# Optimization experiments

Hardware: AMD Instinct MI355X
Metric: run time of the kernel (lower is better)

The kernel has to match this reference:

```python
import jax, jax.numpy as jnp
import numpy as np

# edge types from metadata: (src_type, 'to', dst_type)
NODE_SRC = [0, 1, 2, 3, 0, 1, 2, 1, 3, 1]
NODE_DST = [0, 1, 2, 3, 1, 0, 1, 2, 1, 3]
N_NODES = 30000
N_EDGES = 400000
HEADS1 = 8


def _han_conv(xs, edges, proj_W, proj_b, att_src, att_dst, k_W, k_b, q, heads):
    """Faithful port of torch_geometric HANConv (eval mode, dropout off)."""
    out_ch = proj_W.shape[-1]
    D = out_ch // heads
    N = xs[0].shape[0]
    # per-node-type projection -> [N, H, D]
    h = [(xs[t] @ proj_W[t] + proj_b[t]).reshape(N, heads, D) for t in range(4)]
    outs = {t: [] for t in range(4)}
    for e in range(10):
        s, d = NODE_SRC[e], NODE_DST[e]
        row, col = edges[e, 0], edges[e, 1]
        a_src = (h[s] * att_src[e]).sum(-1)  # [N, H]
        a_dst = (h[d] * att_dst[e]).sum(-1)  # [N, H]
        alpha = jax.nn.leaky_relu(a_src[row] + a_dst[col], 0.2)  # [E, H]
        # segment softmax over incoming edges of each dst node
        amax = jax.ops.segment_max(alpha, col, num_segments=N)
        ex = jnp.exp(alpha - amax[col])
        denom = jax.ops.segment_sum(ex, col, num_segments=N)
        w = ex / (denom[col] + 1e-16)
        msg = h[s][row] * w[:, :, None]  # [E, H, D]
        agg = jax.ops.segment_sum(msg, col, num_segments=N).reshape(N, out_ch)
        outs[d].append(jax.nn.relu(agg))
    # semantic-level attention fusion across relations ending at each node type
    res = []
    for t in range(4):
        stk = jnp.stack(outs[t])  # [M, N, C]
        score = (q * jnp.tanh(stk @ k_W + k_b).mean(axis=1)).sum(-1)  # [M]
        sattn = jax.nn.softmax(score)
        res.append((sattn[:, None, None] * stk).sum(0))  # [N, C]
    return res


def setup_inputs() -> dict:
    key = jax.random.key(0)
    ks = jax.random.split(key, 24)
    inp = {}
    for t in range(4):
        inp[f"x{t}"] = jax.random.normal(ks[t], (N_NODES, 256), dtype=jnp.float32)
    inp["edges"] = jax.random.randint(ks[4], (10, 2, N_EDGES), 0, N_NODES, dtype=jnp.int32)
    s = 0.05
    inp["proj1_W"] = jax.random.normal(ks[5], (4, 256, 128), dtype=jnp.float32) * s
    inp["proj1_b"] = jax.random.normal(ks[6], (4, 128), dtype=jnp.float32) * s
    inp["att1_src"] = jax.random.normal(ks[7], (10, 8, 16), dtype=jnp.float32) * s
    inp["att1_dst"] = jax.random.normal(ks[8], (10, 8, 16), dtype=jnp.float32) * s
    inp["k1_W"] = jax.random.normal(ks[9], (128, 128), dtype=jnp.float32) * s
    inp["k1_b"] = jax.random.normal(ks[10], (128,), dtype=jnp.float32) * s
    inp["q1"] = jax.random.normal(ks[11], (128,), dtype=jnp.float32) * s
    inp["proj2_W"] = jax.random.normal(ks[12], (4, 128, 32), dtype=jnp.float32) * s
    inp["proj2_b"] = jax.random.normal(ks[13], (4, 32), dtype=jnp.float32) * s
    inp["att2_src"] = jax.random.normal(ks[14], (10, 1, 32), dtype=jnp.float32) * s
    inp["att2_dst"] = jax.random.normal(ks[15], (10, 1, 32), dtype=jnp.float32) * s
    inp["k2_W"] = jax.random.normal(ks[16], (32, 32), dtype=jnp.float32) * s
    inp["k2_b"] = jax.random.normal(ks[17], (32,), dtype=jnp.float32) * s
    inp["q2"] = jax.random.normal(ks[18], (32,), dtype=jnp.float32) * s
    return inp


def reference(x0, x1, x2, x3, edges,
              proj1_W, proj1_b, att1_src, att1_dst, k1_W, k1_b, q1,
              proj2_W, proj2_b, att2_src, att2_dst, k2_W, k2_b, q2):
    # eval mode: all F.dropout calls are identity
    xs = [x0, x1, x2, x3]
    h = _han_conv(xs, edges, proj1_W, proj1_b, att1_src, att1_dst, k1_W, k1_b, q1, HEADS1)
    h = [jax.nn.elu(v) for v in h]
    o = _han_conv(h, edges, proj2_W, proj2_b, att2_src, att2_dst, k2_W, k2_b, q2, 1)
    # final per-node softmax over channel dim for each node type; stack since all N equal
    return jnp.stack([jax.nn.softmax(v, axis=1) for v in o])  # [4, N, 32]
```

## Files before the change

### kernel.cpp

```cpp
#include <hip/hip_runtime.h>
#include <hip/hip_fp16.h>

#define NN 30000
#define NE 400000
#define NBUCK 59
#define BPR 98
#define EPB 4096
#define CAPREG 12288
#define BCAP 12288

__constant__ int d_SRC[10] = {0,1,2,3,0,1,2,1,3,1};
__constant__ int d_DST[10] = {0,1,2,3,1,0,1,2,1,3};
__constant__ int d_RORD[10] = {1,5,7,9,0,4,2,6,3,8};
__constant__ int d_FCNT[4] = {2,4,2,2};
__constant__ int d_FREL[4][4] = {{0,5,0,0},{1,4,6,8},{2,7,0,0},{3,9,0,0}};

__constant__ int d_XRELA[8]  = {0,4,2,6,8,1,5,7};
__constant__ int d_XBASEA[8] = {0,1875,3750,5625,0,1875,3750,5625};
__constant__ int d_XCNTA[8]  = {7500,5625,3750,1875,7500,5625,3750,1875};
__constant__ int d_XRELB[8]  = {4,2,6,3,1,5,7,9};

typedef _Float16 f16x8 __attribute__((ext_vector_type(8)));
typedef float f32x4 __attribute__((ext_vector_type(4)));

struct __attribute__((aligned(8))) h2x2 { __half2 a, b; };

template<int BN, bool AF16>
__global__ __launch_bounds__(256)
void mgemm_k(const float* __restrict__ A, long sA,
             const float* __restrict__ B, long sB,
             const float* __restrict__ bias, long sBias,
             float* __restrict__ C, long sC,
             int M, int K, int N, int relu_a, int epi)
{
    constexpr int BM = 128, BK = 32, MR = 2;
    constexpr int NF = BN / 16;
    constexpr int LDK = BK + 8;
    const int z = blockIdx.z;
    const _Float16* __restrict__ Ah = (const _Float16*)A;
    if constexpr (AF16) Ah += (long)z * sA; else A += (long)z * sA;
    B += (long)z * sB;
    bias += (long)z * sBias;
    C += (long)z * sC;
    const int m0 = blockIdx.x * BM;
    const int n0 = blockIdx.y * BN;
    const int tid = threadIdx.x;
    const int wv = tid >> 6;
    const int l  = tid & 63;
    const int fm = l & 15;
    const int fg = l >> 4;

    __shared__ _Float16 As[BM][LDK];
    __shared__ _Float16 Bs[BN][LDK];
    __shared__ float red[4][BN];

    f32x4 acc[MR][NF];
#pragma unroll
    for (int mr = 0; mr < MR; ++mr)
#pragma unroll
        for (int f = 0; f < NF; ++f) acc[mr][f] = (f32x4){0.f, 0.f, 0.f, 0.f};

    const int arow = tid >> 1;
    const int akc  = (tid & 1) << 4;
    const int grow = m0 + arow;

    for (int k0 = 0; k0 < K; k0 += BK) {
        f16x8 ap0, ap1;
        if (grow < M) {
            if constexpr (AF16) {
                const _Float16* aq = Ah + (long)grow * K + k0 + akc;
                ap0 = *(const f16x8*)aq;
                ap1 = *(const f16x8*)(aq + 8);
                if (relu_a) {
#pragma unroll
                    for (int j = 0; j < 8; ++j) {
                        ap0[j] = ap0[j] > (_Float16)0.f ? ap0[j] : (_Float16)0.f;
                        ap1[j] = ap1[j] > (_Float16)0.f ? ap1[j] : (_Float16)0.f;
                    }
                }
            } else {
                const float* aq = A + (long)grow * K + k0 + akc;
                float4 u0 = *(const float4*)aq;
                float4 u1 = *(const float4*)(aq + 4);
                float4 u2 = *(const float4*)(aq + 8);
                float4 u3 = *(const float4*)(aq + 12);
                float v[16] = {u0.x,u0.y,u0.z,u0.w, u1.x,u1.y,u1.z,u1.w,
                               u2.x,u2.y,u2.z,u2.w, u3.x,u3.y,u3.z,u3.w};
                if (relu_a) {
#pragma unroll
                    for (int j = 0; j < 16; ++j) v[j] = fmaxf(v[j], 0.f);
                }
#pragma unroll
                for (int j = 0; j < 8; ++j) { ap0[j] = (_Float16)v[j]; ap1[j] = (_Float16)v[j+8]; }
            }
        } else {
#pragma unroll
            for (int j = 0; j < 8; ++j) { ap0[j] = (_Float16)0.f; ap1[j] = (_Float16)0.f; }
        }
        *(f16x8*)&As[arow][akc]     = ap0;
        *(f16x8*)&As[arow][akc + 8] = ap1;

        if constexpr (BN == 64) {
            const int bk = tid >> 4;
            const int bn = (tid & 15) << 2;
#pragma unroll
            for (int kk = 0; kk < 2; ++kk) {
                int kr = bk + kk * 16;
                float4 u = *(const float4*)(B + (long)(k0 + kr) * N + n0 + bn);
                Bs[bn + 0][kr] = (_Float16)u.x;
                Bs[bn + 1][kr] = (_Float16)u.y;
                Bs[bn + 2][kr] = (_Float16)u.z;
                Bs[bn + 3][kr] = (_Float16)u.w;
            }
        } else {
            const int bk = tid >> 3;
            const int bn = (tid & 7) << 2;
            float4 u = *(const float4*)(B + (long)(k0 + bk) * N + n0 + bn);
            Bs[bn + 0][bk] = (_Float16)u.x;
            Bs[bn + 1][bk] = (_Float16)u.y;
            Bs[bn + 2][bk] = (_Float16)u.z;
            Bs[bn + 3][bk] = (_Float16)u.w;
        }
        __syncthreads();

        f16x8 a0 = *(const f16x8*)&As[wv * 32 + fm][fg * 8];
        f16x8 a1 = *(const f16x8*)&As[wv * 32 + 16 + fm][fg * 8];
#pragma unroll
        for (int f = 0; f < NF; ++f) {
            f16x8 b = *(const f16x8*)&Bs[f * 16 + fm][fg * 8];
            acc[0][f] = __builtin_amdgcn_mfma_f32_16x16x32_f16(a0, b, acc[0][f], 0, 0, 0);
            acc[1][f] = __builtin_amdgcn_mfma_f32_16x16x32_f16(a1, b, acc[1][f], 0, 0, 0);
        }
        __syncthreads();
    }

    if (epi == 0) {
#pragma unroll
        for (int f = 0; f < NF; ++f) {
            float bz = bias[n0 + f * 16 + fm];
#pragma unroll
            for (int mr = 0; mr < MR; ++mr)
#pragma unroll
                for (int i = 0; i < 4; ++i) {
                    int gr = m0 + wv * 32 + mr * 16 + fg * 4 + i;
                    if (gr < M) C[(long)gr * N + n0 + f * 16 + fm] = acc[mr][f][i] + bz;
                }
        }
    } else if (epi == 2) {
        __half* Ch = (__half*)C;
#pragma unroll
        for (int f = 0; f < NF; ++f) {
            float bz = bias[n0 + f * 16 + fm];
#pragma unroll
            for (int mr = 0; mr < MR; ++mr)
#pragma unroll
                for (int i = 0; i < 4; ++i) {
                    int gr = m0 + wv * 32 + mr * 16 + fg * 4 + i;
                    if (gr < M) Ch[(long)gr * N + n0 + f * 16 + fm] = __float2half(acc[mr][f][i] + bz);
                }
        }
    } else {
#pragma unroll
        for (int f = 0; f < NF; ++f) {
            float bz = bias[n0 + f * 16 + fm];
            float s = 0.f;
#pragma unroll
            for (int mr = 0; mr < MR; ++mr)
#pragma unroll
                for (int i = 0; i < 4; ++i) {
                    int gr = m0 + wv * 32 + mr * 16 + fg * 4 + i;
                    if (gr < M) s += tanhf(acc[mr][f][i] + bz);
                }
            s += __shfl_xor(s, 16, 64);
            s += __shfl_xor(s, 32, 64);
            if (fg == 0) red[wv][f * 16 + fm] = s;
        }
        __syncthreads();
        if (tid < BN) {
            float s = red[0][tid] + red[1][tid] + red[2][tid] + red[3][tid];
            unsafeAtomicAdd(&C[n0 + tid], s);
        }
    }
}

__global__ __launch_bounds__(256)
void init_bincur(int* __restrict__ binCur)
{
    int i = blockIdx.x * 256 + threadIdx.x;
    if (i < 10 * NBUCK) binCur[i] = (i % NBUCK) * CAPREG;
}

__global__ __launch_bounds__(256)
void csr_binA(const int* __restrict__ edges, int* __restrict__ binCur,
              unsigned* __restrict__ binned)
{
    __shared__ int lcnt[NBUCK];
    __shared__ int gbase[NBUCK];
    int rel = blockIdx.x / BPR;
    int blk = blockIdx.x - rel * BPR;
    int base = blk * EPB;
    int tid = threadIdx.x;
    for (int b = tid; b < NBUCK; b += 256) lcnt[b] = 0;
    __syncthreads();
    const int* er = edges + (long)rel * 2 * NE;
    const int* ec = er + NE;
    unsigned pk[16];
    unsigned mt[16];
#pragma unroll
    for (int k = 0; k < 16; ++k) {
        int i = base + k * 256 + tid;
        if (i < NE) {
            int r = er[i];
            int c = ec[i];
            int b = c >> 9;
            int lo = atomicAdd(&lcnt[b], 1);
            pk[k] = ((unsigned)c << 15) | (unsigned)r;
            mt[k] = ((unsigned)b << 16) | (unsigned)lo;
        } else {
            mt[k] = 0xFFFFFFFFu;
        }
    }
    __syncthreads();
    if (tid < NBUCK) gbase[tid] = atomicAdd(&binCur[rel * NBUCK + tid], lcnt[tid]);
    __syncthreads();
    unsigned* bn = binned + (long)rel * NBUCK * CAPREG;
#pragma unroll
    for (int k = 0; k < 16; ++k) {
        if (mt[k] != 0xFFFFFFFFu) {
            int b = mt[k] >> 16;
            int lo = mt[k] & 0xFFFF;
            bn[gbase[b] + lo] = pk[k];
        }
    }
}

__global__ __launch_bounds__(64)
void bucket_scan(const int* __restrict__ binCur, int* __restrict__ bbase,
                 int* __restrict__ off_all)
{
    int rel = blockIdx.x;
    int t = threadIdx.x;
    __shared__ int c[64];
    int v = (t < NBUCK) ? (binCur[rel * NBUCK + t] - t * CAPREG) : 0;
    c[t] = v;
    __syncthreads();
    for (int d = 1; d < 64; d <<= 1) {
        int u = (t >= d) ? c[t - d] : 0;
        __syncthreads();
        c[t] += u;
        __syncthreads();
    }
    if (t < NBUCK) bbase[rel * NBUCK + t] = c[t] - v;
    if (t == 0) off_all[rel * (NN + 1) + NN] = NE;
}

__global__ __launch_bounds__(256)
void csr_binB(const int* __restrict__ binCur, const int* __restrict__ bbase,
              const unsigned* __restrict__ binned,
              int* __restrict__ off_all, unsigned short* __restrict__ rows)
{
    __shared__ int cntS[512];
    __shared__ int lcur[512];
    __shared__ int part[256];
    __shared__ int buf[BCAP];
    int rel = blockIdx.x / NBUCK;
    int bkt = blockIdx.x - rel * NBUCK;
    const unsigned* bn = binned + ((long)rel * NBUCK + bkt) * CAPREG;
    int* off = off_all + rel * (NN + 1);
    unsigned short* rw = rows + (long)rel * NE;
    int cnt = binCur[rel * NBUCK + bkt] - bkt * CAPREG;
    int gbase = bbase[rel * NBUCK + bkt];
    int nb0 = bkt << 9;
    int nb1 = min(nb0 + 512, NN);
    int nloc = nb1 - nb0;
    int tid = threadIdx.x;

    cntS[tid] = 0; cntS[tid + 256] = 0;
    __syncthreads();
    for (int j = tid; j < cnt; j += 256) {
        int c = (int)(bn[j] >> 15);
        atomicAdd(&cntS[c - nb0], 1);
    }
    __syncthreads();
    int c0 = cntS[2 * tid], c1 = cntS[2 * tid + 1];
    part[tid] = c0 + c1;
    __syncthreads();
    for (int d = 1; d < 256; d <<= 1) {
        int u = (tid >= d) ? part[tid - d] : 0;
        __syncthreads();
        part[tid] += u;
        __syncthreads();
    }
    int pre = (tid == 0) ? 0 : part[tid - 1];
    cntS[2 * tid] = pre;
    cntS[2 * tid + 1] = pre + c0;
    __syncthreads();
    for (int i = tid; i < nloc; i += 256) off[nb0 + i] = gbase + cntS[i];
    lcur[tid] = cntS[tid]; lcur[tid + 256] = cntS[tid + 256];
    __syncthreads();
    if (cnt <= BCAP) {
        for (int j = tid; j < cnt; j += 256) {
            unsigned p = bn[j];
            int r = (int)(p & 0x7FFF);
            int c = (int)(p >> 15);
            int pos = atomicAdd(&lcur[c - nb0], 1);
            buf[pos] = r;
        }
        __syncthreads();
        for (int i = tid; i < cnt; i += 256) rw[gbase + i] = (unsigned short)buf[i];
    } else {
        for (int j = tid; j < cnt; j += 256) {
            unsigned p = bn[j];
            int r = (int)(p & 0x7FFF);
            int c = (int)(p >> 15);
            int pos = atomicAdd(&lcur[c - nb0], 1);
            rw[gbase + pos] = (unsigned short)r;
        }
    }
}

__global__ __launch_bounds__(256)
void attn_dots1(const __half* __restrict__ h1h,
                const float* __restrict__ att_src,
                const float* __restrict__ att_dst,
                float* __restrict__ asrc, float* __restrict__ adst)
{
    int gid = blockIdx.x * 256 + threadIdx.x;
    int wave = gid >> 6;
    int lane = gid & 63;
    if (wave >= 4 * NN) return;
    int t = wave / NN;
    int n = wave - t * NN;
    __half2 hh = *(const __half2*)&h1h[(long)(t * NN + n) * 128 + 2 * lane];
    float2 hv = __half22float2(hh);
    const int SRCc[10] = {0,1,2,3,0,1,2,1,3,1};
    const int DSTc[10] = {0,1,2,3,1,0,1,2,1,3};
#pragma unroll
    for (int e = 0; e < 10; ++e) {
        if (SRCc[e] == t) {
            float2 av = *(const float2*)&att_src[e * 128 + 2 * lane];
            float p = hv.x * av.x + hv.y * av.y;
#pragma unroll
            for (int off = 1; off < 8; off <<= 1) p += __shfl_xor(p, off, 64);
            if ((lane & 7) == 0) asrc[(long)(e * NN + n) * 8 + (lane >> 3)] = p;
        }
        if (DSTc[e] == t) {
            float2 bv = *(const float2*)&att_dst[e * 128 + 2 * lane];
            float p = hv.x * bv.x + hv.y * bv.y;
#pragma unroll
            for (int off = 1; off < 8; off <<= 1) p += __shfl_xor(p, off, 64);
            if ((lane & 7) == 0) adst[(long)(e * NN + n) * 8 + (lane >> 3)] = p;
        }
    }
}

__global__ __launch_bounds__(256)
void gather_agg1_all(const int* __restrict__ csr_off,
                     const unsigned short* __restrict__ csr_rows,
                     const float* __restrict__ asrc1, const float* __restrict__ adst1,
                     const __half* __restrict__ h1h, __half* __restrict__ slots16)
{
    int g = blockIdx.x;
    int xcd = g & 7;
    int slot = g >> 3;
    int e, i;
    if (slot < d_XCNTA[xcd]) { e = d_XRELA[xcd]; i = d_XBASEA[xcd] + slot; }
    else                     { e = d_XRELB[xcd]; i = slot - d_XCNTA[xcd]; }
    int node = i * 4 + (threadIdx.x >> 6);
    int lane = threadIdx.x & 63;
    if (node >= NN) return;
    const int* off = csr_off + e * (NN + 1);
    const unsigned short* rows = csr_rows + (long)e * NE;
    const float* asrc_e = asrc1 + (long)e * NN * 8;
    const float* adst_e = adst1 + (long)e * NN * 8;
    const _Float16* h1s = (const _Float16*)h1h + (long)d_SRC[e] * NN * 128;
    __half* out = slots16 + (long)e * NN * 128;

    const int g2  = lane >> 4;
    const int s16 = lane & 15;
    const int hv  = s16 >> 1;
    const int eA  = lane >> 3;
    const int hA  = lane & 7;
    int beg = off[node], end = off[node + 1];
    float adA = adst_e[node * 8 + hA];
    float den = (g2 == 0) ? 1e-16f : 0.f;
    float a0 = 0.f, a1 = 0.f, a2 = 0.f, a3 = 0.f;
    float a4 = 0.f, a5 = 0.f, a6 = 0.f, a7 = 0.f;

#define GA1_STEP(i)                                                              \
    {                                                                            \
        int e0 = 4 * (i) + g2;                                                   \
        float wi = __shfl(w, e0 * 8 + hv, 64);                                   \
        int ri = __shfl(r, e0 * 8, 64);                                          \
        f16x8 v = *(const f16x8*)(h1s + (long)ri * 128 + 8 * s16);               \
        den += wi;                                                               \
        a0 += wi * (float)v[0]; a1 += wi * (float)v[1];                          \
        a2 += wi * (float)v[2]; a3 += wi * (float)v[3];                          \
        a4 += wi * (float)v[4]; a5 += wi * (float)v[5];                          \
        a6 += wi * (float)v[6]; a7 += wi * (float)v[7];                          \
    }

    if (beg < end) {
        int j0 = beg;
        int jj = j0 + eA;
        bool ok = jj < end;
        int r = (int)rows[ok ? jj : beg];
        float aw = asrc_e[r * 8 + hA] + adA;
        while (true) {
            float al = aw > 0.f ? aw : 0.2f * aw;
            float w = ok ? __expf(al) : 0.f;
            int j1 = j0 + 8;
            int rn = r; float awn = 0.f; bool okn = false;
            if (j1 < end) {
                int jn = j1 + eA;
                okn = jn < end;
                rn = (int)rows[okn ? jn : beg];
                awn = asrc_e[rn * 8 + hA] + adA;
            }
            int cnt = end - j0;
            GA1_STEP(0)
            if (cnt > 4) { GA1_STEP(1) }
            if (j1 >= end) break;
            j0 = j1; r = rn; aw = awn; ok = okn;
        }
    }
#undef GA1_STEP
#pragma unroll
    for (int m = 16; m < 64; m <<= 1) {
        a0 += __shfl_xor(a0, m, 64); a1 += __shfl_xor(a1, m, 64);
        a2 += __shfl_xor(a2, m, 64); a3 += __shfl_xor(a3, m, 64);
        a4 += __shfl_xor(a4, m, 64); a5 += __shfl_xor(a5, m, 64);
        a6 += __shfl_xor(a6, m, 64); a7 += __shfl_xor(a7, m, 64);
        den += __shfl_xor(den, m, 64);
    }
    if (g2 == 0) {
        float inv = 1.0f / den;
        f16x8 o;
        o[0] = (_Float16)(a0 * inv); o[1] = (_Float16)(a1 * inv);
        o[2] = (_Float16)(a2 * inv); o[3] = (_Float16)(a3 * inv);
        o[4] = (_Float16)(a4 * inv); o[5] = (_Float16)(a5 * inv);
        o[6] = (_Float16)(a6 * inv); o[7] = (_Float16)(a7 * inv);
        *(f16x8*)((_Float16*)out + (long)node * 128 + 8 * s16) = o;
    }
}

__global__ __launch_bounds__(256)
void fusion_all(const __half* __restrict__ slots16, const float* __restrict__ sattn,
                __half* __restrict__ h1f)
{
    int t = blockIdx.y;
    int idx = blockIdx.x * 256 + threadIdx.x;
    if (idx >= NN * 32) return;
    int c4 = idx & 31;
    int n = idx >> 5;
    long off = (long)n * 128 + c4 * 4;
    int cnt = d_FCNT[t];
    float o0 = 0.f, o1 = 0.f, o2 = 0.f, o3 = 0.f;
    for (int j = 0; j < cnt; ++j) {
        int e = d_FREL[t][j];
        float w = sattn[e];
        const __half* p = slots16 + (long)e * NN * 128 + off;
        float2 v01 = __half22float2(*(const __half2*)p);
        float2 v23 = __half22float2(*(const __half2*)(p + 2));
        o0 += w * fmaxf(v01.x, 0.f);
        o1 += w * fmaxf(v01.y, 0.f);
        o2 += w * fmaxf(v23.x, 0.f);
        o3 += w * fmaxf(v23.y, 0.f);
    }
    o0 = o0 > 0.f ? o0 : __expf(o0) - 1.f;
    o1 = o1 > 0.f ? o1 : __expf(o1) - 1.f;
    o2 = o2 > 0.f ? o2 : __expf(o2) - 1.f;
    o3 = o3 > 0.f ? o3 : __expf(o3) - 1.f;
    __half* q = h1f + (long)t * NN * 128 + off;
    *(__half2*)q = __floats2half2_rn(o0, o1);
    *(__half2*)(q + 2) = __floats2half2_rn(o2, o3);
}

__global__ __launch_bounds__(256)
void attn_dots2(const __half* __restrict__ h2h,
                const float* __restrict__ att_src,
                const float* __restrict__ att_dst,
                float* __restrict__ asrc, float* __restrict__ adst)
{
    int gid = blockIdx.x * 256 + threadIdx.x;
    int p = gid >> 5;
    int l = gid & 31;
    if (p >= 10 * NN) return;
    int e = p / NN, n = p - e * NN;
    int s = d_SRC[e], d = d_DST[e];
    float hs = __half2float(h2h[(long)(s * NN + n) * 32 + l]);
    float hd = __half2float(h2h[(long)(d * NN + n) * 32 + l]);
    float ps = hs * att_src[e * 32 + l];
    float pd = hd * att_dst[e * 32 + l];
#pragma unroll
    for (int off = 1; off < 32; off <<= 1) {
        ps += __shfl_xor(ps, off, 64);
        pd += __shfl_xor(pd, off, 64);
    }
    if (l == 0) { asrc[e * NN + n] = ps; adst[e * NN + n] = pd; }
}

__global__ __launch_bounds__(256)
void gather_agg2(const int* __restrict__ csr_off,
                 const unsigned short* __restrict__ csr_rows,
                 const __half* __restrict__ h2h,
                 const float* __restrict__ asrc, const float* __restrict__ adst,
                 __half* __restrict__ agg2h)
{
    int e = d_RORD[blockIdx.y];
    int node = blockIdx.x * 8 + (threadIdx.x >> 5);
    int lane = threadIdx.x & 31;
    if (node >= NN) return;
    const int* off = csr_off + e * (NN + 1);
    const unsigned short* rows = csr_rows + (long)e * NE;
    const __half* h2s = h2h + (long)d_SRC[e] * NN * 32;
    const float* as = asrc + e * NN;
    const int slot = lane >> 3;
    const int sub = lane & 7;
    float ad = adst[e * NN + node];
    int beg = off[node], end = off[node + 1];
    float den = (slot == 0) ? 1e-16f : 0.f;
    float a0 = 0.f, a1 = 0.f, a2 = 0.f, a3 = 0.f;

#define GA2_STEP(i)                                                              \
    {                                                                            \
        int e0 = (i) * 4 + slot;                                                 \
        float wi = __shfl(w, e0, 32);                                            \
        int ri = __shfl(r, e0, 32);                                              \
        h2x2 v = *(const h2x2*)(h2s + (long)ri * 32 + 4 * sub);                  \
        float2 f0 = __half22float2(v.a);                                         \
        float2 f1 = __half22float2(v.b);                                         \
        den += wi;                                                               \
        a0 += wi * f0.x; a1 += wi * f0.y; a2 += wi * f1.x; a3 += wi * f1.y;      \
    }

    for (int j0 = beg; j0 < end; j0 += 32) {
        int jj = j0 + lane;
        bool ok = jj < end;
        int r = (int)rows[ok ? jj : beg];
        float a = as[r] + ad;
        a = a > 0.f ? a : 0.2f * a;
        float w = ok ? __expf(a) : 0.f;
        int cnt = end - j0;
        if (cnt >= 32) {
            GA2_STEP(0) GA2_STEP(1) GA2_STEP(2) GA2_STEP(3)
            GA2_STEP(4) GA2_STEP(5) GA2_STEP(6) GA2_STEP(7)
        } else {
            int it = (cnt + 3) >> 2;
            for (int i = 0; i < it; ++i) GA2_STEP(i)
        }
    }
#undef GA2_STEP
#pragma unroll
    for (int m = 8; m < 32; m <<= 1) {
        a0 += __shfl_xor(a0, m, 32);
        a1 += __shfl_xor(a1, m, 32);
        a2 += __shfl_xor(a2, m, 32);
        a3 += __shfl_xor(a3, m, 32);
        den += __shfl_xor(den, m, 32);
    }
    if (slot == 0) {
        float inv = 1.0f / den;
        h2x2 o;
        o.a = __floats2half2_rn(a0 * inv, a1 * inv);
        o.b = __floats2half2_rn(a2 * inv, a3 * inv);
        *(h2x2*)(agg2h + ((long)e * NN + node) * 32 + 4 * sub) = o;
    }
}

__global__ void score_all_k(const float* __restrict__ colsum, const float* __restrict__ q,
                            float* __restrict__ sattn, int C)
{
    __shared__ float sc[10];
    int tid = threadIdx.x;
    if (tid < 10) {
        float s = 0.f;
        for (int c = 0; c < C; ++c) s += q[c] * colsum[tid * C + c];
        sc[tid] = s / (float)NN;
    }
    __syncthreads();
    if (tid < 4) {
        float mx = -1e30f;
        for (int m = 0; m < 10; ++m) if (d_DST[m] == tid) mx = fmaxf(mx, sc[m]);
        float ex[10];
        float sum = 0.f;
        for (int m = 0; m < 10; ++m) {
            ex[m] = 0.f;
            if (d_DST[m] == tid) { ex[m] = __expf(sc[m] - mx); sum += ex[m]; }
        }
        for (int m = 0; m < 10; ++m) if (d_DST[m] == tid) sattn[m] = ex[m] / sum;
    }
}

__global__ __launch_bounds__(256)
void final_softmax(const __half* __restrict__ agg, const float* __restrict__ sattn,
                   float* __restrict__ out)
{
    int gid = blockIdx.x * 256 + threadIdx.x;
    int c = gid & 31;
    int p = gid >> 5;
    if (p >= 4 * NN) return;
    int t = p / NN, n = p - t * NN;
    float f = 0.f;
    for (int m = 0; m < 10; ++m) {
        if (d_DST[m] != t) continue;
        f += sattn[m] * fmaxf(__half2float(agg[(long)(m * NN + n) * 32 + c]), 0.f);
    }
    float mx = f;
#pragma unroll
    for (int off = 1; off < 32; off <<= 1) mx = fmaxf(mx, __shfl_xor(mx, off, 64));
    float ex = __expf(f - mx);
    float sm = ex;
#pragma unroll
    for (int off = 1; off < 32; off <<= 1) sm += __shfl_xor(sm, off, 64);
    out[(long)(t * NN + n) * 32 + c] = ex / sm;
}

extern "C" void kernel_launch(void* const* d_in, const int* in_sizes, int n_in,
                              void* d_out, int out_size, void* d_ws, size_t ws_size,
                              hipStream_t stream) {
    const float* x[4] = {
        (const float*)d_in[0], (const float*)d_in[1],
        (const float*)d_in[2], (const float*)d_in[3]};
    const int* edges = (const int*)d_in[4];
    const float* W1    = (const float*)d_in[5];
    const float* b1    = (const float*)d_in[6];
    const float* att1s = (const float*)d_in[7];
    const float* att1d = (const float*)d_in[8];
    const float* k1W   = (const float*)d_in[9];
    const float* k1b   = (const float*)d_in[10];
    const float* q1    = (const float*)d_in[11];
    const float* W2    = (const float*)d_in[12];
    const float* b2    = (const float*)d_in[13];
    const float* att2s = (const float*)d_in[14];
    const float* att2d = (const float*)d_in[15];
    const float* k2W   = (const float*)d_in[16];
    const float* k2b   = (const float*)d_in[17];
    const float* q2    = (const float*)d_in[18];

    float* W = (float*)d_ws;
    __half* h1h    = (__half*)W;
    __half* h1f    = (__half*)W;
    __half* h2h    = (__half*)(W + 7680000);
    __half* slots16 = (__half*)(W + 15360000);
    __half* agg2h  = (__half*)(W + 15360000);
    unsigned* binned = (unsigned*)(W + 15360000);
    int*   binCur  = (int*)(W + 15360000 + 7249920);
    int*   bbase   = binCur + 640;
    float* asrc1   = W + 34560000;
    float* adst1   = W + 36960000;
    float* asrc2   = W + 36960000;
    float* adst2   = W + 37260000;
    float* colsum1 = W + 39360000;
    float* sattn1  = W + 39361280;
    float* colsum2 = W + 39361296;
    float* sattn2  = W + 39361616;
    int*   csr_off = (int*)(W + 39361640);
    unsigned short* csr_row = (unsigned short*)(csr_off + 300016);

    init_bincur<<<3, 256, 0, stream>>>(binCur);
    csr_binA<<<BPR * 10, 256, 0, stream>>>(edges, binCur, binned);
    bucket_scan<<<10, 64, 0, stream>>>(binCur, bbase, csr_off);
    csr_binB<<<NBUCK * 10, 256, 0, stream>>>(binCur, bbase, binned, csr_off, csr_row);

    hipMemsetAsync(colsum1, 0, 1632L * 4, stream);

    for (int t = 0; t < 4; ++t) {
        mgemm_k<64, false><<<dim3(235, 2, 1), 256, 0, stream>>>(
            x[t], 0, W1 + (long)t * 256 * 128, 0, b1 + t * 128, 0,
            (float*)(h1h + (long)t * NN * 128), 0, NN, 256, 128, 0, 2);
    }

    attn_dots1<<<30000, 256, 0, stream>>>(h1h, att1s, att1d, asrc1, adst1);

    gather_agg1_all<<<75000, 256, 0, stream>>>(
        csr_off, csr_row, asrc1, adst1, h1h, slots16);

    mgemm_k<64, true><<<dim3(235, 2, 10), 256, 0, stream>>>(
        (const float*)slots16, (long)NN * 128, k1W, 0, k1b, 0,
        colsum1, 128, NN, 128, 128, 1, 1);
    score_all_k<<<1, 64, 0, stream>>>(colsum1, q1, sattn1, 128);

    fusion_all<<<dim3(3750, 4), 256, 0, stream>>>(slots16, sattn1, h1f);

    mgemm_k<32, true><<<dim3(235, 1, 4), 256, 0, stream>>>(
        (const float*)h1f, (long)NN * 128, W2, 128L * 32, b2, 32,
        (float*)h2h, (long)NN * 16, NN, 128, 32, 0, 2);

    attn_dots2<<<37500, 256, 0, stream>>>(h2h, att2s, att2d, asrc2, adst2);
    gather_agg2<<<dim3(3750, 10), 256, 0, stream>>>(
        csr_off, csr_row, h2h, asrc2, adst2, agg2h);

    mgemm_k<32, true><<<dim3(235, 1, 10), 256, 0, stream>>>(
        (const float*)agg2h, (long)NN * 32, k2W, 0, k2b, 0,
        colsum2, 32L, NN, 32, 32, 1, 1);
    score_all_k<<<1, 64, 0, stream>>>(colsum2, q2, sattn2, 32);
    final_softmax<<<15000, 256, 0, stream>>>(agg2h, sattn2, (float*)d_out);
}
```

Before: 762.3 us.

## Merge setup kernels, batch layer-1 projection, split CSR rows by source half

Several changes land together. The layer-1 projection becomes one batched launch over all four node types instead of four launches. The bucket_scan kernel and the memset are folded into csr_binB and a combined init kernel. CSR rows within each destination are partitioned into low and high source indices, with a split offset stored per node. The layer-1 gather then walks the two segments separately, dropping its software-prefetch loop, presumably to improve locality of the h1 row gathers. This removes several launches, but each csr_binB block now recomputes the prefix sum serially and the gather loses its prefetch overlap.

Result: faster. 728.5 us (-4.4%).

```diff
diff --git a/kernel.cpp b/kernel.cpp
--- a/kernel.cpp
+++ b/kernel.cpp
@@ -8,6 +8,7 @@
 #define EPB 4096
 #define CAPREG 12288
 #define BCAP 12288
+#define HSPLIT 15000
 
 __constant__ int d_SRC[10] = {0,1,2,3,0,1,2,1,3,1};
 __constant__ int d_DST[10] = {0,1,2,3,1,0,1,2,1,3};
@@ -25,9 +26,101 @@
 
 struct __attribute__((aligned(8))) h2x2 { __half2 a, b; };
 
-template<int BN, bool AF16>
-__global__ __launch_bounds__(256)
-void mgemm_k(const float* __restrict__ A, long sA,
+__global__ __launch_bounds__(256)
+void proj1_k(const float* __restrict__ A0, const float* __restrict__ A1,
+             const float* __restrict__ A2, const float* __restrict__ A3,
+             const float* __restrict__ B, const float* __restrict__ bias,
+             __half* __restrict__ C)
+{
+    constexpr int BM = 128, BK = 32, MR = 2, NF = 4, LDK = BK + 8;
+    constexpr int K = 256, N = 128, M = NN;
+    const int z = blockIdx.z;
+    const float* A = (z == 0) ? A0 : (z == 1) ? A1 : (z == 2) ? A2 : A3;
+    const float* Bz = B + (long)z * K * N;
+    const float* bz = bias + z * N;
+    __half* Cz = C + (long)z * M * N;
+    const int m0 = blockIdx.x * BM;
+    const int n0 = blockIdx.y * 64;
+    const int tid = threadIdx.x;
+    const int wv = tid >> 6;
+    const int l  = tid & 63;
+    const int fm = l & 15;
+    const int fg = l >> 4;
+
+    __shared__ _Float16 As[BM][LDK];
+    __shared__ _Float16 Bs[64][LDK];
+
+    f32x4 acc[MR][NF];
+#pragma unroll
+    for (int mr = 0; mr < MR; ++mr)
+#pragma unroll
+        for (int f = 0; f < NF; ++f) acc[mr][f] = (f32x4){0.f, 0.f, 0.f, 0.f};
+
+    const int arow = tid >> 1;
+    const int akc  = (tid & 1) << 4;
+    const int grow = m0 + arow;
+
+    for (int k0 = 0; k0 < K; k0 += BK) {
+        f16x8 ap0, ap1;
+        if (grow < M) {
+            const float* aq = A + (long)grow * K + k0 + akc;
+            float4 u0 = *(const float4*)aq;
+            float4 u1 = *(const float4*)(aq + 4);
+            float4 u2 = *(const float4*)(aq + 8);
+            float4 u3 = *(const float4*)(aq + 12);
+            float v[16] = {u0.x,u0.y,u0.z,u0.w, u1.x,u1.y,u1.z,u1.w,
+                           u2.x,u2.y,u2.z,u2.w, u3.x,u3.y,u3.z,u3.w};
+#pragma unroll
+            for (int j = 0; j < 8; ++j) { ap0[j] = (_Float16)v[j]; ap1[j] = (_Float16)v[j+8]; }
+        } else {
+#pragma unroll
+            for (int j = 0; j < 8; ++j) { ap0[j] = (_Float16)0.f; ap1[j] = (_Float16)0.f; }
+        }
+        *(f16x8*)&As[arow][akc]     = ap0;
+        *(f16x8*)&As[arow][akc + 8] = ap1;
+
+        {
+            const int bk = tid >> 4;
+            const int bn = (tid & 15) << 2;
+#pragma unroll
+            for (int kk = 0; kk < 2; ++kk) {
+                int kr = bk + kk * 16;
+                float4 u = *(const float4*)(Bz + (long)(k0 + kr) * N + n0 + bn);
+                Bs[bn + 0][kr] = (_Float16)u.x;
+                Bs[bn + 1][kr] = (_Float16)u.y;
+                Bs[bn + 2][kr] = (_Float16)u.z;
+                Bs[bn + 3][kr] = (_Float16)u.w;
+            }
+        }
+        __syncthreads();
+
+        f16x8 a0 = *(const f16x8*)&As[wv * 32 + fm][fg * 8];
+        f16x8 a1 = *(const f16x8*)&As[wv * 32 + 16 + fm][fg * 8];
+#pragma unroll
+        for (int f = 0; f < NF; ++f) {
+            f16x8 b = *(const f16x8*)&Bs[f * 16 + fm][fg * 8];
+            acc[0][f] = __builtin_amdgcn_mfma_f32_16x16x32_f16(a0, b, acc[0][f], 0, 0, 0);
+            acc[1][f] = __builtin_amdgcn_mfma_f32_16x16x32_f16(a1, b, acc[1][f], 0, 0, 0);
+        }
+        __syncthreads();
+    }
+
+#pragma unroll
+    for (int f = 0; f < NF; ++f) {
+        float bzv = bz[n0 + f * 16 + fm];
+#pragma unroll
+        for (int mr = 0; mr < MR; ++mr)
+#pragma unroll
+            for (int i = 0; i < 4; ++i) {
+                int gr = m0 + wv * 32 + mr * 16 + fg * 4 + i;
+                if (gr < M) Cz[(long)gr * N + n0 + f * 16 + fm] = __float2half(acc[mr][f][i] + bzv);
+            }
+    }
+}
+
+template<int BN>
+__global__ __launch_bounds__(256)
+void mgemm_k(const _Float16* __restrict__ Ah, long sA,
              const float* __restrict__ B, long sB,
              const float* __restrict__ bias, long sBias,
              float* __restrict__ C, long sC,
@@ -37,8 +130,7 @@
     constexpr int NF = BN / 16;
     constexpr int LDK = BK + 8;
     const int z = blockIdx.z;
-    const _Float16* __restrict__ Ah = (const _Float16*)A;
-    if constexpr (AF16) Ah += (long)z * sA; else A += (long)z * sA;
+    Ah += (long)z * sA;
     B += (long)z * sB;
     bias += (long)z * sBias;
     C += (long)z * sC;
@@ -67,31 +159,15 @@
     for (int k0 = 0; k0 < K; k0 += BK) {
         f16x8 ap0, ap1;
         if (grow < M) {
-            if constexpr (AF16) {
-                const _Float16* aq = Ah + (long)grow * K + k0 + akc;
-                ap0 = *(const f16x8*)aq;
-                ap1 = *(const f16x8*)(aq + 8);
-                if (relu_a) {
-#pragma unroll
-                    for (int j = 0; j < 8; ++j) {
-                        ap0[j] = ap0[j] > (_Float16)0.f ? ap0[j] : (_Float16)0.f;
-                        ap1[j] = ap1[j] > (_Float16)0.f ? ap1[j] : (_Float16)0.f;
-                    }
+            const _Float16* aq = Ah + (long)grow * K + k0 + akc;
+            ap0 = *(const f16x8*)aq;
+            ap1 = *(const f16x8*)(aq + 8);
+            if (relu_a) {
+#pragma unroll
+                for (int j = 0; j < 8; ++j) {
+                    ap0[j] = ap0[j] > (_Float16)0.f ? ap0[j] : (_Float16)0.f;
+                    ap1[j] = ap1[j] > (_Float16)0.f ? ap1[j] : (_Float16)0.f;
                 }
-            } else {
-                const float* aq = A + (long)grow * K + k0 + akc;
-                float4 u0 = *(const float4*)aq;
-                float4 u1 = *(const float4*)(aq + 4);
-                float4 u2 = *(const float4*)(aq + 8);
-                float4 u3 = *(const float4*)(aq + 12);
-                float v[16] = {u0.x,u0.y,u0.z,u0.w, u1.x,u1.y,u1.z,u1.w,
-                               u2.x,u2.y,u2.z,u2.w, u3.x,u3.y,u3.z,u3.w};
-                if (relu_a) {
-#pragma unroll
-                    for (int j = 0; j < 16; ++j) v[j] = fmaxf(v[j], 0.f);
-                }
-#pragma unroll
-                for (int j = 0; j < 8; ++j) { ap0[j] = (_Float16)v[j]; ap1[j] = (_Float16)v[j+8]; }
             }
         } else {
 #pragma unroll
@@ -134,19 +210,7 @@
         __syncthreads();
     }
 
-    if (epi == 0) {
-#pragma unroll
-        for (int f = 0; f < NF; ++f) {
-            float bz = bias[n0 + f * 16 + fm];
-#pragma unroll
-            for (int mr = 0; mr < MR; ++mr)
-#pragma unroll
-                for (int i = 0; i < 4; ++i) {
-                    int gr = m0 + wv * 32 + mr * 16 + fg * 4 + i;
-                    if (gr < M) C[(long)gr * N + n0 + f * 16 + fm] = acc[mr][f][i] + bz;
-                }
-        }
-    } else if (epi == 2) {
+    if (epi == 2) {
         __half* Ch = (__half*)C;
 #pragma unroll
         for (int f = 0; f < NF; ++f) {
@@ -184,10 +248,11 @@
 }
 
 __global__ __launch_bounds__(256)
-void init_bincur(int* __restrict__ binCur)
+void init_k(int* __restrict__ binCur, float* __restrict__ colsum)
 {
     int i = blockIdx.x * 256 + threadIdx.x;
     if (i < 10 * NBUCK) binCur[i] = (i % NBUCK) * CAPREG;
+    if (i < 1632) colsum[i] = 0.f;
 }
 
 __global__ __launch_bounds__(256)
@@ -234,52 +299,41 @@
     }
 }
 
-__global__ __launch_bounds__(64)
-void bucket_scan(const int* __restrict__ binCur, int* __restrict__ bbase,
-                 int* __restrict__ off_all)
-{
-    int rel = blockIdx.x;
-    int t = threadIdx.x;
-    __shared__ int c[64];
-    int v = (t < NBUCK) ? (binCur[rel * NBUCK + t] - t * CAPREG) : 0;
-    c[t] = v;
-    __syncthreads();
-    for (int d = 1; d < 64; d <<= 1) {
-        int u = (t >= d) ? c[t - d] : 0;
-        __syncthreads();
-        c[t] += u;
-        __syncthreads();
-    }
-    if (t < NBUCK) bbase[rel * NBUCK + t] = c[t] - v;
-    if (t == 0) off_all[rel * (NN + 1) + NN] = NE;
-}
-
-__global__ __launch_bounds__(256)
-void csr_binB(const int* __restrict__ binCur, const int* __restrict__ bbase,
-              const unsigned* __restrict__ binned,
-              int* __restrict__ off_all, unsigned short* __restrict__ rows)
+__global__ __launch_bounds__(256)
+void csr_binB(const int* __restrict__ binCur, const unsigned* __restrict__ binned,
+              int* __restrict__ off_all, unsigned short* __restrict__ rows,
+              int* __restrict__ splits)
 {
     __shared__ int cntS[512];
+    __shared__ int cntL[512];
     __shared__ int lcur[512];
+    __shared__ int hcur[512];
     __shared__ int part[256];
     __shared__ int buf[BCAP];
     int rel = blockIdx.x / NBUCK;
     int bkt = blockIdx.x - rel * NBUCK;
     const unsigned* bn = binned + ((long)rel * NBUCK + bkt) * CAPREG;
     int* off = off_all + rel * (NN + 1);
+    int* spl = splits + rel * NN;
     unsigned short* rw = rows + (long)rel * NE;
     int cnt = binCur[rel * NBUCK + bkt] - bkt * CAPREG;
-    int gbase = bbase[rel * NBUCK + bkt];
+    int gbase = 0;
+    for (int b = 0; b < bkt; ++b) gbase += binCur[rel * NBUCK + b] - b * CAPREG;
     int nb0 = bkt << 9;
     int nb1 = min(nb0 + 512, NN);
     int nloc = nb1 - nb0;
     int tid = threadIdx.x;
+    if (bkt == 0 && tid == 0) off[NN] = NE;
 
     cntS[tid] = 0; cntS[tid + 256] = 0;
+    cntL[tid] = 0; cntL[tid + 256] = 0;
     __syncthreads();
     for (int j = tid; j < cnt; j += 256) {
-        int c = (int)(bn[j] >> 15);
+        unsigned p = bn[j];
+        int c = (int)(p >> 15);
+        int r = (int)(p & 0x7FFF);
         atomicAdd(&cntS[c - nb0], 1);
+        if (r < HSPLIT) atomicAdd(&cntL[c - nb0], 1);
     }
     __syncthreads();
     int c0 = cntS[2 * tid], c1 = cntS[2 * tid + 1];
@@ -295,15 +349,20 @@
     cntS[2 * tid] = pre;
     cntS[2 * tid + 1] = pre + c0;
     __syncthreads();
-    for (int i = tid; i < nloc; i += 256) off[nb0 + i] = gbase + cntS[i];
-    lcur[tid] = cntS[tid]; lcur[tid + 256] = cntS[tid + 256];
+    for (int i = tid; i < nloc; i += 256) {
+        off[nb0 + i] = gbase + cntS[i];
+        spl[nb0 + i] = gbase + cntS[i] + cntL[i];
+    }
+    lcur[tid] = cntS[tid];               lcur[tid + 256] = cntS[tid + 256];
+    hcur[tid] = cntS[tid] + cntL[tid];   hcur[tid + 256] = cntS[tid + 256] + cntL[tid + 256];
     __syncthreads();
     if (cnt <= BCAP) {
         for (int j = tid; j < cnt; j += 256) {
             unsigned p = bn[j];
             int r = (int)(p & 0x7FFF);
             int c = (int)(p >> 15);
-            int pos = atomicAdd(&lcur[c - nb0], 1);
+            int pos = (r < HSPLIT) ? atomicAdd(&lcur[c - nb0], 1)
+                                   : atomicAdd(&hcur[c - nb0], 1);
             buf[pos] = r;
         }
         __syncthreads();
@@ -313,7 +372,8 @@
             unsigned p = bn[j];
             int r = (int)(p & 0x7FFF);
             int c = (int)(p >> 15);
-            int pos = atomicAdd(&lcur[c - nb0], 1);
+            int pos = (r < HSPLIT) ? atomicAdd(&lcur[c - nb0], 1)
+                                   : atomicAdd(&hcur[c - nb0], 1);
             rw[gbase + pos] = (unsigned short)r;
         }
     }
@@ -355,7 +415,7 @@
 }
 
 __global__ __launch_bounds__(256)
-void gather_agg1_all(const int* __restrict__ csr_off,
+void gather_agg1_all(const int* __restrict__ csr_off, const int* __restrict__ splits,
                      const unsigned short* __restrict__ csr_rows,
                      const float* __restrict__ asrc1, const float* __restrict__ adst1,
                      const __half* __restrict__ h1h, __half* __restrict__ slots16)
@@ -370,6 +430,7 @@
     int lane = threadIdx.x & 63;
     if (node >= NN) return;
     const int* off = csr_off + e * (NN + 1);
+    const int* spl = splits + e * NN;
     const unsigned short* rows = csr_rows + (long)e * NE;
     const float* asrc_e = asrc1 + (long)e * NN * 8;
     const float* adst_e = adst1 + (long)e * NN * 8;
@@ -382,6 +443,7 @@
     const int eA  = lane >> 3;
     const int hA  = lane & 7;
     int beg = off[node], end = off[node + 1];
+    int mid = spl[node];
     float adA = adst_e[node * 8 + hA];
     float den = (g2 == 0) ? 1e-16f : 0.f;
     float a0 = 0.f, a1 = 0.f, a2 = 0.f, a3 = 0.f;
@@ -400,28 +462,20 @@
         a6 += wi * (float)v[6]; a7 += wi * (float)v[7];                          \
     }
 
-    if (beg < end) {
-        int j0 = beg;
-        int jj = j0 + eA;
-        bool ok = jj < end;
-        int r = (int)rows[ok ? jj : beg];
-        float aw = asrc_e[r * 8 + hA] + adA;
-        while (true) {
+#pragma unroll 1
+    for (int seg = 0; seg < 2; ++seg) {
+        int s0 = seg ? mid : beg;
+        int s1 = seg ? end : mid;
+        for (int j0 = s0; j0 < s1; j0 += 8) {
+            int jj = j0 + eA;
+            bool ok = jj < s1;
+            int r = (int)rows[ok ? jj : s0];
+            float aw = asrc_e[r * 8 + hA] + adA;
             float al = aw > 0.f ? aw : 0.2f * aw;
             float w = ok ? __expf(al) : 0.f;
-            int j1 = j0 + 8;
-            int rn = r; float awn = 0.f; bool okn = false;
-            if (j1 < end) {
-                int jn = j1 + eA;
-                okn = jn < end;
-                rn = (int)rows[okn ? jn : beg];
-                awn = asrc_e[rn * 8 + hA] + adA;
-            }
-            int cnt = end - j0;
+            int cnt = s1 - j0;
             GA1_STEP(0)
             if (cnt > 4) { GA1_STEP(1) }
-            if (j1 >= end) break;
-            j0 = j1; r = rn; aw = awn; ok = okn;
         }
     }
 #undef GA1_STEP
@@ -646,7 +700,6 @@
     __half* agg2h  = (__half*)(W + 15360000);
     unsigned* binned = (unsigned*)(W + 15360000);
     int*   binCur  = (int*)(W + 15360000 + 7249920);
-    int*   bbase   = binCur + 640;
     float* asrc1   = W + 34560000;
     float* adst1   = W + 36960000;
     float* asrc2   = W + 36960000;
@@ -657,42 +710,37 @@
     float* sattn2  = W + 39361616;
     int*   csr_off = (int*)(W + 39361640);
     unsigned short* csr_row = (unsigned short*)(csr_off + 300016);
-
-    init_bincur<<<3, 256, 0, stream>>>(binCur);
+    int*   csr_spl = (int*)(csr_row + 4000000);
+
+    init_k<<<7, 256, 0, stream>>>(binCur, colsum1);
     csr_binA<<<BPR * 10, 256, 0, stream>>>(edges, binCur, binned);
-    bucket_scan<<<10, 64, 0, stream>>>(binCur, bbase, csr_off);
-    csr_binB<<<NBUCK * 10, 256, 0, stream>>>(binCur, bbase, binned, csr_off, csr_row);
-
-    hipMemsetAsync(colsum1, 0, 1632L * 4, stream);
-
-    for (int t = 0; t < 4; ++t) {
-        mgemm_k<64, false><<<dim3(235, 2, 1), 256, 0, stream>>>(
-            x[t], 0, W1 + (long)t * 256 * 128, 0, b1 + t * 128, 0,
-            (float*)(h1h + (long)t * NN * 128), 0, NN, 256, 128, 0, 2);
-    }
+    csr_binB<<<NBUCK * 10, 256, 0, stream>>>(binCur, binned, csr_off, csr_row, csr_spl);
+
+    proj1_k<<<dim3(235, 2, 4), 256, 0, stream>>>(
+        x[0], x[1], x[2], x[3], W1, b1, h1h);
 
     attn_dots1<<<30000, 256, 0, stream>>>(h1h, att1s, att1d, asrc1, adst1);
 
     gather_agg1_all<<<75000, 256, 0, stream>>>(
-        csr_off, csr_row, asrc1, adst1, h1h, slots16);
-
-    mgemm_k<64, true><<<dim3(235, 2, 10), 256, 0, stream>>>(
-        (const float*)slots16, (long)NN * 128, k1W, 0, k1b, 0,
+        csr_off, csr_spl, csr_row, asrc1, adst1, h1h, slots16);
+
+    mgemm_k<64><<<dim3(235, 2, 10), 256, 0, stream>>>(
+        (const _Float16*)slots16, (long)NN * 128, k1W, 0, k1b, 0,
         colsum1, 128, NN, 128, 128, 1, 1);
     score_all_k<<<1, 64, 0, stream>>>(colsum1, q1, sattn1, 128);
 
     fusion_all<<<dim3(3750, 4), 256, 0, stream>>>(slots16, sattn1, h1f);
 
-    mgemm_k<32, true><<<dim3(235, 1, 4), 256, 0, stream>>>(
-        (const float*)h1f, (long)NN * 128, W2, 128L * 32, b2, 32,
+    mgemm_k<32><<<dim3(235, 1, 4), 256, 0, stream>>>(
+        (const _Float16*)h1f, (long)NN * 128, W2, 128L * 32, b2, 32,
         (float*)h2h, (long)NN * 16, NN, 128, 32, 0, 2);
 
     attn_dots2<<<37500, 256, 0, stream>>>(h2h, att2s, att2d, asrc2, adst2);
     gather_agg2<<<dim3(3750, 10), 256, 0, stream>>>(
         csr_off, csr_row, h2h, asrc2, adst2, agg2h);
 
-    mgemm_k<32, true><<<dim3(235, 1, 10), 256, 0, stream>>>(
-        (const float*)agg2h, (long)NN * 32, k2W, 0, k2b, 0,
+    mgemm_k<32><<<dim3(235, 1, 10), 256, 0, stream>>>(
+        (const _Float16*)agg2h, (long)NN * 32, k2W, 0, k2b, 0,
         colsum2, 32L, NN, 32, 32, 1, 1);
     score_all_k<<<1, 64, 0, stream>>>(colsum2, q2, sattn2, 32);
     final_softmax<<<15000, 256, 0, stream>>>(agg2h, sattn2, (float*)d_out);
```
